# Performance work log

Hardware: AMD Instinct MI355X
Metric: run time of the kernel (lower is better)

Reference implementation:

```python
import jax, jax.numpy as jnp
import numpy as np

B, C, D, K = 65536, 128, 32, 10
EPS = 1e-12


def setup_inputs() -> dict:
    key = jax.random.key(0)
    k1, k2, k3, k4 = jax.random.split(key, 4)
    data = jax.random.normal(k1, (B, D), dtype=jnp.float32)
    mu = jax.random.normal(k2, (C, D), dtype=jnp.float32)
    # S_inv must be symmetric positive definite (inverse covariance per cluster)
    A = 0.1 * jax.random.normal(k3, (C, D, D), dtype=jnp.float32)
    S_inv = jnp.einsum('cij,ckj->cik', A, A) + jnp.eye(D, dtype=jnp.float32)[None]
    # one-hot class assignment per cluster (int32), as stored in the module
    cls = jax.random.randint(k4, (C,), 0, K)
    cluster_labels = jax.nn.one_hot(cls, K, dtype=jnp.int32)
    return {"data": data, "mu": mu, "S_inv": S_inv, "cluster_labels": cluster_labels}


def reference(data, mu, S_inv, cluster_labels):
    # Mahalanobis distance d2[b,c] = (z_b - mu_c)^T S_inv_c (z_b - mu_c),
    # expanded to avoid a [B, C, D] diff tensor.
    zz = data[:, :, None] * data[:, None, :]            # [B, D, D]
    t1 = jnp.einsum('bde,cde->bc', zz, S_inv)           # z' Sinv z
    Sm = jnp.einsum('cde,ce->cd', S_inv, mu)            # [C, D]
    t2 = data @ Sm.T                                    # z' Sinv mu  [B, C]
    t3 = jnp.einsum('cd,cd->c', mu, Sm)                 # mu' Sinv mu [C]
    d2 = t1 - 2.0 * t2 + t3[None, :]                    # [B, C]
    Gamma = jnp.exp(-0.5 * d2)                          # Gaussian activation
    # defuzzify_batch: normalize activations, project through one-hot labels
    norm_gamma = Gamma / (jnp.sum(Gamma, axis=1, keepdims=True) + EPS)
    label_scores = norm_gamma @ cluster_labels.astype(jnp.float32)  # [B, K]
    preds = jnp.argmax(label_scores, axis=1)
    clusters = jnp.argmax(Gamma, axis=1)
    return label_scores, preds, clusters
```

## Files before the change

### kernel.cpp

```cpp
#include <hip/hip_runtime.h>
#include <cmath>

#define B_N 65536
#define C_N 128
#define D_N 32
#define K_N 10
#define EPS_F 1e-12f
#define SCALE_F (-0.72134752044448169f)

#define NKK 48
#define CHUNK_F16 4096
#define QF_N (NKK * CHUNK_F16)
#define YSTR 33

typedef _Float16 f16x8 __attribute__((ext_vector_type(8)));
typedef float    f32x16 __attribute__((ext_vector_type(16)));

__device__ __forceinline__ void mdkk(int kk, int& dA, int& e0) {
    if (kk >= 45) { dA = 0; e0 = 0; return; }
    int w = (kk >= 17) + (kk >= 30) + (kk >= 39) + (kk >= 44);
    int off = w == 0 ? 0 : (w == 1 ? 17 : (w == 2 ? 30 : (w == 3 ? 39 : 44)));
    int r = kk - off;
    dA = 2 * r;
    e0 = 2 * r + 8 * w;
}

__global__ __launch_bounds__(128) void k_prep(const float* __restrict__ S,
                                              const float* __restrict__ mu,
                                              const int* __restrict__ onehot,
                                              _Float16* __restrict__ QF,
                                              int* __restrict__ cls) {
    const int c = blockIdx.x;
    const int tid = threadIdx.x;
    __shared__ float sSm[D_N];
    __shared__ float st3;

    if (tid < D_N) {
        const float* Sr = S + (size_t)c * (D_N * D_N) + (size_t)tid * D_N;
        const float* mr = mu + (size_t)c * D_N;
        float a0 = 0.f, a1 = 0.f;
#pragma unroll
        for (int e = 0; e < D_N; e += 2) {
            a0 = fmaf(Sr[e + 0], mr[e + 0], a0);
            a1 = fmaf(Sr[e + 1], mr[e + 1], a1);
        }
        sSm[tid] = a0 + a1;
    }
    __syncthreads();
    if (tid == 0) {
        const float* mr = mu + (size_t)c * D_N;
        float a = 0.f;
#pragma unroll
        for (int d = 0; d < D_N; ++d) a = fmaf(mr[d], sSm[d], a);
        st3 = a;
        int cl = 0;
#pragma unroll
        for (int k = 0; k < K_N; ++k)
            if (onehot[c * K_N + k] != 0) cl = k;
        cls[c] = cl;
    }
    __syncthreads();

    if (tid < 2 * NKK) {
        const int kk   = tid >> 1;
        const int half = tid & 1;
        int dA, e0;
        mdkk(kk, dA, e0);
        const int d  = dA + half;
        const int ct = c >> 5;
        const size_t base = (size_t)kk * CHUNK_F16 + ct * 1024
                          + (size_t)(half * 32 + (c & 31)) * 8;
        const float* Sc = S + (size_t)c * (D_N * D_N);
        for (int j = 0; j < 8; ++j) {
            const int e = e0 + j;
            float q = 0.f;
            if (kk < 45 && d <= e && e <= 32) {
                float v;
                if (e < 32)      v = Sc[d * D_N + e] * (d == e ? 1.f : 2.f);
                else if (d < 32) v = -2.f * sSm[d];
                else             v = st3;
                q = SCALE_F * v;
            }
            _Float16 h = (_Float16)q;
            QF[base + j]       = h;
            QF[base + 512 + j] = (_Float16)(q - (float)h);
        }
    }
}

__device__ __forceinline__ void gl_lds16(const void* g, void* l) {
    __builtin_amdgcn_global_load_lds(
        (const __attribute__((address_space(1))) unsigned int*)g,
        (__attribute__((address_space(3))) unsigned int*)l, 16, 0, 0);
}

__device__ __forceinline__ void mkphi(float yd, const float (&yw)[8],
                                      f16x8& ph, f16x8& pl) {
    union { unsigned int w[4]; f16x8 v; } H, L;
#pragma unroll
    for (int p = 0; p < 4; ++p) {
        float f0 = yd * yw[2 * p], f1 = yd * yw[2 * p + 1];
        auto h2 = __builtin_amdgcn_cvt_pkrtz(f0, f1);
        float r0 = f0 - (float)h2[0];
        float r1 = f1 - (float)h2[1];
        auto l2 = __builtin_amdgcn_cvt_pkrtz(r0, r1);
        __builtin_memcpy(&H.w[p], &h2, 4);
        __builtin_memcpy(&L.w[p], &l2, 4);
    }
    ph = H.v;
    pl = L.v;
}

__global__ __launch_bounds__(512, 4) void k_mainv10(const float* __restrict__ data,
                                                    const _Float16* __restrict__ QF,
                                                    const int* __restrict__ clsp,
                                                    float* __restrict__ out) {
    const int tid  = threadIdx.x;
    const int lane = tid & 63;
    const int wid  = tid >> 6;
    const int rg   = wid >> 1;
    const int cg   = wid & 1;
    const int col  = lane & 31;
    const bool hi  = lane >= 32;
    const int bb   = blockIdx.x * 128;

    __shared__ float sy[128 * YSTR + 64];
    __shared__ alignas(16) _Float16 qb[4 * CHUNK_F16];
    __shared__ int lcls[C_N];
    __shared__ float scr[4][2][32][14];

    if (tid < C_N) lcls[tid] = clsp[tid];
    if (tid < 128) {
        const float4* p0 = (const float4*)(data + (size_t)(bb + tid) * D_N);
        const int yb = tid * YSTR;
#pragma unroll
        for (int i = 0; i < 8; ++i) {
            float4 v = p0[i];
            sy[yb + 4 * i + 0] = v.x;
            sy[yb + 4 * i + 1] = v.y;
            sy[yb + 4 * i + 2] = v.z;
            sy[yb + 4 * i + 3] = v.w;
        }
        sy[yb + 32] = 1.f;
    } else if (tid < 192) {
        sy[128 * YSTR + (tid - 128)] = 0.f;
    }

    f32x16 acc[2];
#pragma unroll
    for (int lt = 0; lt < 2; ++lt)
#pragma unroll
        for (int g = 0; g < 16; ++g) acc[lt][g] = 0.f;

    gl_lds16(QF + 0 * CHUNK_F16 + wid * 512 + lane * 8, qb + 0 * CHUNK_F16 + wid * 512);
    gl_lds16(QF + 1 * CHUNK_F16 + wid * 512 + lane * 8, qb + 1 * CHUNK_F16 + wid * 512);
    __syncthreads();

    const int hioff = hi ? 1 : 0;
    const float* yrow = sy + (rg * 32 + col) * YSTR;
    float yw[8], yd = 0.f;
    int e0 = 0, dAh = hioff;

#pragma clang loop unroll(disable)
    for (int t = 0; t < NKK; ++t) {
        asm volatile("s_waitcnt vmcnt(0)" ::: "memory");
        __builtin_amdgcn_s_barrier();
        __builtin_amdgcn_sched_barrier(0);
        if (t + 2 < NKK)
            gl_lds16(QF + (size_t)(t + 2) * CHUNK_F16 + wid * 512 + lane * 8,
                     qb + ((t + 2) & 3) * CHUNK_F16 + wid * 512);

        if (t == 0 || t == 17 || t == 30 || t == 39 || t == 44) {
            e0  = (t == 0) ? 0 : (t == 17) ? 8 : (t == 30) ? 16 : (t == 39) ? 24 : 32;
            dAh = hioff;
#pragma unroll
            for (int j = 0; j < 8; ++j) yw[j] = yrow[e0 + j];
            yd = yrow[dAh];
        } else if (t < 45) {
            e0 += 2; dAh += 2;
            yw[0] = yw[2]; yw[1] = yw[3]; yw[2] = yw[4];
            yw[3] = yw[5]; yw[4] = yw[6]; yw[5] = yw[7];
            yw[6] = yrow[e0 + 6];
            yw[7] = yrow[e0 + 7];
            yd = yrow[dAh];
        }

        const f16x8* qc = (const f16x8*)(qb + ((t & 3) * CHUNK_F16) + cg * 2048);
        f16x8 qh0 = qc[lane],       ql0 = qc[64 + lane];
        f16x8 qh1 = qc[128 + lane], ql1 = qc[192 + lane];

        f16x8 ph, pl;
        mkphi(yd, yw, ph, pl);
        __builtin_amdgcn_s_setprio(1);
        acc[0] = __builtin_amdgcn_mfma_f32_32x32x16_f16(qh0, ph, acc[0], 0, 0, 0);
        acc[1] = __builtin_amdgcn_mfma_f32_32x32x16_f16(qh1, ph, acc[1], 0, 0, 0);
        acc[0] = __builtin_amdgcn_mfma_f32_32x32x16_f16(ql0, ph, acc[0], 0, 0, 0);
        acc[1] = __builtin_amdgcn_mfma_f32_32x32x16_f16(ql1, ph, acc[1], 0, 0, 0);
        acc[0] = __builtin_amdgcn_mfma_f32_32x32x16_f16(qh0, pl, acc[0], 0, 0, 0);
        acc[1] = __builtin_amdgcn_mfma_f32_32x32x16_f16(qh1, pl, acc[1], 0, 0, 0);
        __builtin_amdgcn_s_setprio(0);
    }

    const float hoff = hi ? 4.f : 0.f;
    const int* lc = lcls + (hi ? 4 : 0);
    float sum = 0.f, gmax = -1.f, gcf = 0.f;
    float a0 = 0, a1 = 0, a2 = 0, a3 = 0, a4 = 0, a5 = 0, a6 = 0, a7 = 0, a8 = 0, a9 = 0;
#pragma unroll
    for (int lt = 0; lt < 2; ++lt) {
        const int gt = cg * 2 + lt;
        float psum = 0.f;
#pragma unroll
        for (int g = 0; g < 16; ++g) {
            float v = acc[lt][g];
            float gm;
            asm("v_exp_f32 %0, %1" : "=v"(gm) : "v"(v));
            const int cbase = gt * 32 + (g & 3) + 8 * (g >> 2);
            int cl = lc[cbase];
            psum += gm;
            float cf = (float)cbase + hoff;
            if (gm > gmax) { gmax = gm; gcf = cf; }
            a0 += (cl == 0) ? gm : 0.f;
            a1 += (cl == 1) ? gm : 0.f;
            a2 += (cl == 2) ? gm : 0.f;
            a3 += (cl == 3) ? gm : 0.f;
            a4 += (cl == 4) ? gm : 0.f;
            a5 += (cl == 5) ? gm : 0.f;
            a6 += (cl == 6) ? gm : 0.f;
            a7 += (cl == 7) ? gm : 0.f;
            a8 += (cl == 8) ? gm : 0.f;
            a9 += (cl == 9) ? gm : 0.f;
        }
        sum += psum;
    }

    sum += __shfl_xor(sum, 32, 64);
    {
        float om = __shfl_xor(gmax, 32, 64);
        float oc = __shfl_xor(gcf, 32, 64);
        bool take = (om > gmax) || (om == gmax && oc < gcf);
        if (take) { gmax = om; gcf = oc; }
    }
    a0 += __shfl_xor(a0, 32, 64);
    a1 += __shfl_xor(a1, 32, 64);
    a2 += __shfl_xor(a2, 32, 64);
    a3 += __shfl_xor(a3, 32, 64);
    a4 += __shfl_xor(a4, 32, 64);
    a5 += __shfl_xor(a5, 32, 64);
    a6 += __shfl_xor(a6, 32, 64);
    a7 += __shfl_xor(a7, 32, 64);
    a8 += __shfl_xor(a8, 32, 64);
    a9 += __shfl_xor(a9, 32, 64);

    if (!hi) {
        float* s = scr[rg][cg][col];
        s[0] = sum; s[1] = gmax; s[2] = gcf;
        s[3] = a0; s[4] = a1; s[5] = a2; s[6] = a3; s[7] = a4;
        s[8] = a5; s[9] = a6; s[10] = a7; s[11] = a8; s[12] = a9;
    }
    __syncthreads();

    if (cg == 0 && !hi) {
        const float* s0 = scr[rg][0][col];
        const float* s1 = scr[rg][1][col];
        float fs = s0[0] + s1[0];
        float gm = s0[1];
        float gc = s0[2];
        if (s1[1] > gm) { gm = s1[1]; gc = s1[2]; }
        float inv = 1.0f / (fs + EPS_F);
        float ls[K_N];
        float best = -1.f;
        int bk = 0;
#pragma unroll
        for (int k = 0; k < K_N; ++k) {
            ls[k] = (s0[3 + k] + s1[3 + k]) * inv;
            if (ls[k] > best) { best = ls[k]; bk = k; }
        }
        const int b = bb + rg * 32 + col;
        float2* o2 = (float2*)(out + (size_t)b * K_N);
#pragma unroll
        for (int k2 = 0; k2 < K_N / 2; ++k2)
            o2[k2] = make_float2(ls[2 * k2], ls[2 * k2 + 1]);
        out[(size_t)B_N * K_N + b] = (float)bk;
        out[(size_t)B_N * K_N + B_N + b] = gc;
    }
}

extern "C" void kernel_launch(void* const* d_in, const int* in_sizes, int n_in,
                              void* d_out, int out_size, void* d_ws, size_t ws_size,
                              hipStream_t stream) {
    const float* data   = (const float*)d_in[0];
    const float* mu     = (const float*)d_in[1];
    const float* S      = (const float*)d_in[2];
    const int*   onehot = (const int*)d_in[3];
    float* out = (float*)d_out;

    _Float16* QF  = (_Float16*)d_ws;
    int*      cls = (int*)(QF + QF_N);

    hipLaunchKernelGGL(k_prep, dim3(C_N), dim3(128), 0, stream,
                       S, mu, onehot, QF, cls);
    hipLaunchKernelGGL(k_mainv10, dim3(B_N / 128), dim3(512), 0, stream,
                       data, QF, cls, out);
}
```

Baseline: 110.3 us.

## Load Q coefficients directly from global into registers, drop LDS staging and barriers

Replaces the LDS ring buffer, which was filled through global_load_lds with a per-iteration barrier, with per-wave register double buffering. Each wave loads its Q fragments straight from global memory (through L2/L1). The loop is unrolled by two and stops at the 45 live k-steps instead of 48, so the padding iterations are skipped. This removes the per-step block-wide barrier and frees LDS for occupancy. In exchange, every wave re-reads the same Q data from cache, which adds VGPR pressure and exposes global-load latency.

```diff
diff --git a/kernel.cpp b/kernel.cpp
--- a/kernel.cpp
+++ b/kernel.cpp
@@ -9,6 +9,7 @@
 #define SCALE_F (-0.72134752044448169f)
 
 #define NKK 48
+#define NLIVE 45
 #define CHUNK_F16 4096
 #define QF_N (NKK * CHUNK_F16)
 #define YSTR 33
@@ -88,10 +89,15 @@
     }
 }
 
-__device__ __forceinline__ void gl_lds16(const void* g, void* l) {
-    __builtin_amdgcn_global_load_lds(
-        (const __attribute__((address_space(1))) unsigned int*)g,
-        (__attribute__((address_space(3))) unsigned int*)l, 16, 0, 0);
+__device__ __forceinline__ void ldq_g(const f16x8* __restrict__ qg,
+                                      int t, int cg, int lane,
+                                      f16x8& qh0, f16x8& ql0,
+                                      f16x8& qh1, f16x8& ql1) {
+    const f16x8* p = qg + (size_t)t * 512 + cg * 256 + lane;
+    qh0 = p[0];
+    ql0 = p[64];
+    qh1 = p[128];
+    ql1 = p[192];
 }
 
 __device__ __forceinline__ void mkphi(float yd, const float (&yw)[8],
@@ -111,7 +117,42 @@
     pl = L.v;
 }
 
-__global__ __launch_bounds__(512, 4) void k_mainv10(const float* __restrict__ data,
+__device__ __forceinline__ void ystep(const float* __restrict__ yrow, int hioff,
+                                      int t, int& e0, int& dAh,
+                                      float& yd, float (&yw)[8]) {
+    if (t == 0 || t == 17 || t == 30 || t == 39 || t == 44) {
+        e0  = (t == 0) ? 0 : (t == 17) ? 8 : (t == 30) ? 16 : (t == 39) ? 24 : 32;
+        dAh = hioff;
+#pragma unroll
+        for (int j = 0; j < 8; ++j) yw[j] = yrow[e0 + j];
+        yd = yrow[dAh];
+    } else {
+        e0 += 2; dAh += 2;
+        yw[0] = yw[2]; yw[1] = yw[3]; yw[2] = yw[4];
+        yw[3] = yw[5]; yw[4] = yw[6]; yw[5] = yw[7];
+        yw[6] = yrow[e0 + 6];
+        yw[7] = yrow[e0 + 7];
+        yd = yrow[dAh];
+    }
+}
+
+__device__ __forceinline__ void do6(const f16x8& qh0, const f16x8& ql0,
+                                    const f16x8& qh1, const f16x8& ql1,
+                                    float yd, const float (&yw)[8],
+                                    f32x16 (&acc)[2]) {
+    f16x8 ph, pl;
+    mkphi(yd, yw, ph, pl);
+    __builtin_amdgcn_s_setprio(1);
+    acc[0] = __builtin_amdgcn_mfma_f32_32x32x16_f16(qh0, ph, acc[0], 0, 0, 0);
+    acc[1] = __builtin_amdgcn_mfma_f32_32x32x16_f16(qh1, ph, acc[1], 0, 0, 0);
+    acc[0] = __builtin_amdgcn_mfma_f32_32x32x16_f16(ql0, ph, acc[0], 0, 0, 0);
+    acc[1] = __builtin_amdgcn_mfma_f32_32x32x16_f16(ql1, ph, acc[1], 0, 0, 0);
+    acc[0] = __builtin_amdgcn_mfma_f32_32x32x16_f16(qh0, pl, acc[0], 0, 0, 0);
+    acc[1] = __builtin_amdgcn_mfma_f32_32x32x16_f16(qh1, pl, acc[1], 0, 0, 0);
+    __builtin_amdgcn_s_setprio(0);
+}
+
+__global__ __launch_bounds__(512, 4) void k_mainv11(const float* __restrict__ data,
                                                     const _Float16* __restrict__ QF,
                                                     const int* __restrict__ clsp,
                                                     float* __restrict__ out) {
@@ -125,7 +166,6 @@
     const int bb   = blockIdx.x * 128;
 
     __shared__ float sy[128 * YSTR + 64];
-    __shared__ alignas(16) _Float16 qb[4 * CHUNK_F16];
     __shared__ int lcls[C_N];
     __shared__ float scr[4][2][32][14];
 
@@ -145,6 +185,7 @@
     } else if (tid < 192) {
         sy[128 * YSTR + (tid - 128)] = 0.f;
     }
+    __syncthreads();
 
     f32x16 acc[2];
 #pragma unroll
@@ -152,54 +193,26 @@
 #pragma unroll
         for (int g = 0; g < 16; ++g) acc[lt][g] = 0.f;
 
-    gl_lds16(QF + 0 * CHUNK_F16 + wid * 512 + lane * 8, qb + 0 * CHUNK_F16 + wid * 512);
-    gl_lds16(QF + 1 * CHUNK_F16 + wid * 512 + lane * 8, qb + 1 * CHUNK_F16 + wid * 512);
-    __syncthreads();
-
+    const f16x8* qg = (const f16x8*)QF;
+    const float* yrow = sy + (rg * 32 + col) * YSTR;
     const int hioff = hi ? 1 : 0;
-    const float* yrow = sy + (rg * 32 + col) * YSTR;
     float yw[8], yd = 0.f;
     int e0 = 0, dAh = hioff;
 
+    f16x8 Ah0, Al0, Ah1, Al1, Bh0, Bl0, Bh1, Bl1;
+    ldq_g(qg, 0, cg, lane, Ah0, Al0, Ah1, Al1);
+
 #pragma clang loop unroll(disable)
-    for (int t = 0; t < NKK; ++t) {
-        asm volatile("s_waitcnt vmcnt(0)" ::: "memory");
-        __builtin_amdgcn_s_barrier();
-        __builtin_amdgcn_sched_barrier(0);
-        if (t + 2 < NKK)
-            gl_lds16(QF + (size_t)(t + 2) * CHUNK_F16 + wid * 512 + lane * 8,
-                     qb + ((t + 2) & 3) * CHUNK_F16 + wid * 512);
-
-        if (t == 0 || t == 17 || t == 30 || t == 39 || t == 44) {
-            e0  = (t == 0) ? 0 : (t == 17) ? 8 : (t == 30) ? 16 : (t == 39) ? 24 : 32;
-            dAh = hioff;
-#pragma unroll
-            for (int j = 0; j < 8; ++j) yw[j] = yrow[e0 + j];
-            yd = yrow[dAh];
-        } else if (t < 45) {
-            e0 += 2; dAh += 2;
-            yw[0] = yw[2]; yw[1] = yw[3]; yw[2] = yw[4];
-            yw[3] = yw[5]; yw[4] = yw[6]; yw[5] = yw[7];
-            yw[6] = yrow[e0 + 6];
-            yw[7] = yrow[e0 + 7];
-            yd = yrow[dAh];
-        }
-
-        const f16x8* qc = (const f16x8*)(qb + ((t & 3) * CHUNK_F16) + cg * 2048);
-        f16x8 qh0 = qc[lane],       ql0 = qc[64 + lane];
-        f16x8 qh1 = qc[128 + lane], ql1 = qc[192 + lane];
-
-        f16x8 ph, pl;
-        mkphi(yd, yw, ph, pl);
-        __builtin_amdgcn_s_setprio(1);
-        acc[0] = __builtin_amdgcn_mfma_f32_32x32x16_f16(qh0, ph, acc[0], 0, 0, 0);
-        acc[1] = __builtin_amdgcn_mfma_f32_32x32x16_f16(qh1, ph, acc[1], 0, 0, 0);
-        acc[0] = __builtin_amdgcn_mfma_f32_32x32x16_f16(ql0, ph, acc[0], 0, 0, 0);
-        acc[1] = __builtin_amdgcn_mfma_f32_32x32x16_f16(ql1, ph, acc[1], 0, 0, 0);
-        acc[0] = __builtin_amdgcn_mfma_f32_32x32x16_f16(qh0, pl, acc[0], 0, 0, 0);
-        acc[1] = __builtin_amdgcn_mfma_f32_32x32x16_f16(qh1, pl, acc[1], 0, 0, 0);
-        __builtin_amdgcn_s_setprio(0);
-    }
+    for (int t = 0; t < NLIVE - 1; t += 2) {
+        ldq_g(qg, t + 1, cg, lane, Bh0, Bl0, Bh1, Bl1);
+        ystep(yrow, hioff, t, e0, dAh, yd, yw);
+        do6(Ah0, Al0, Ah1, Al1, yd, yw, acc);
+        ldq_g(qg, t + 2, cg, lane, Ah0, Al0, Ah1, Al1);
+        ystep(yrow, hioff, t + 1, e0, dAh, yd, yw);
+        do6(Bh0, Bl0, Bh1, Bl1, yd, yw, acc);
+    }
+    ystep(yrow, hioff, NLIVE - 1, e0, dAh, yd, yw);
+    do6(Ah0, Al0, Ah1, Al1, yd, yw, acc);
 
     const float hoff = hi ? 4.f : 0.f;
     const int* lc = lcls + (hi ? 4 : 0);
@@ -299,6 +312,6 @@
 
     hipLaunchKernelGGL(k_prep, dim3(C_N), dim3(128), 0, stream,
                        S, mu, onehot, QF, cls);
-    hipLaunchKernelGGL(k_mainv10, dim3(B_N / 128), dim3(512), 0, stream,
+    hipLaunchKernelGGL(k_mainv11, dim3(B_N / 128), dim3(512), 0, stream,
                        data, QF, cls, out);
 }
```

Result: slower. 112.8 us (+2.2%).
